# Kernel tuning notes

Hardware: AMD Instinct MI355X
Metric: run time of the kernel (lower is better)

Reference implementation:

```python
import jax, jax.numpy as jnp
import numpy as np
from jax import lax

B, T_DEC, T_ENC = 32, 400, 300
N_MEL, PRENET, ENC_D = 80, 256, 512
ATT_RNN, DEC_RNN, ATT_D = 512, 512, 128
LOC_F, LOC_K = 32, 31


def setup_inputs() -> dict:
    key = jax.random.key(0)
    ks = jax.random.split(key, 24)

    def w(k, shape):
        return jax.random.normal(k, shape, jnp.float32) / np.float32(np.sqrt(shape[-1]))

    inp = {
        "encoder_out": jax.random.normal(ks[0], (B, T_ENC, ENC_D), jnp.float32),
        "mels": jax.random.normal(ks[1], (B, T_DEC, N_MEL), jnp.float32),
        "lengths": jax.random.randint(ks[2], (B,), 1, T_ENC + 1).astype(jnp.int32),
        # prenet (3 layers, no bias)
        "W_p0": w(ks[3], (PRENET, N_MEL)),
        "W_p1": w(ks[4], (PRENET, PRENET)),
        "W_p2": w(ks[5], (PRENET, PRENET)),
        # attention GRUCell: input = prenet_dim + enc_dim = 768
        "W_ih_a": w(ks[6], (3 * ATT_RNN, PRENET + ENC_D)),
        "W_hh_a": w(ks[7], (3 * ATT_RNN, ATT_RNN)),
        "b_ih_a": jnp.zeros((3 * ATT_RNN,), jnp.float32),
        "b_hh_a": jnp.zeros((3 * ATT_RNN,), jnp.float32),
        # decoder GRUCell: input = attn_rnn + enc_dim = 1024 (what the code actually feeds)
        "W_ih_d": w(ks[8], (3 * DEC_RNN, ATT_RNN + ENC_D)),
        "W_hh_d": w(ks[9], (3 * DEC_RNN, DEC_RNN)),
        "b_ih_d": jnp.zeros((3 * DEC_RNN,), jnp.float32),
        "b_hh_d": jnp.zeros((3 * DEC_RNN,), jnp.float32),
        # location-sensitive attention
        "W_q": w(ks[10], (ATT_D, ATT_RNN)),
        "W_m": w(ks[11], (ATT_D, ENC_D)),
        "K_loc": w(ks[12], (LOC_F, 2, LOC_K)),
        "W_l": w(ks[13], (ATT_D, LOC_F)),
        "v": w(ks[14], (ATT_D,)),
        # output projection + gate
        "W_out": w(ks[15], (N_MEL, DEC_RNN + ENC_D)),
        "b_out": jnp.zeros((N_MEL,), jnp.float32),
        "W_g": w(ks[16], (1, DEC_RNN + ENC_D)),
        "b_g": jnp.zeros((1,), jnp.float32),
    }
    return inp


def _gru_cell(x, h, W_ih, W_hh, b_ih, b_hh):
    gi = x @ W_ih.T + b_ih
    gh = h @ W_hh.T + b_hh
    i_r, i_z, i_n = jnp.split(gi, 3, axis=-1)
    h_r, h_z, h_n = jnp.split(gh, 3, axis=-1)
    r = jax.nn.sigmoid(i_r + h_r)
    z = jax.nn.sigmoid(i_z + h_z)
    n = jnp.tanh(i_n + r * h_n)
    return (1.0 - z) * n + z * h


def _decoder_core(encoder_out, mels, lengths, W_p0, W_p1, W_p2,
                  W_ih_a, W_hh_a, b_ih_a, b_hh_a, W_ih_d, W_hh_d, b_ih_d, b_hh_d,
                  W_q, W_m, K_loc, W_l, v, W_out, b_out, W_g, b_g):
    Bb, T_enc, _ = encoder_out.shape
    T_dec = mels.shape[1]
    pmem = encoder_out @ W_m.T  # [B,T_enc,ATT_D], computed once
    enc_mask = jnp.arange(T_enc)[None, :] < lengths[:, None]  # [B,T_enc]
    # shifted teacher-forcing inputs: zero first frame, then mels[:, :-1]
    dec_inputs = jnp.concatenate(
        [jnp.zeros((Bb, 1, mels.shape[2]), mels.dtype), mels[:, :-1]], axis=1)
    drop_key = jax.random.key(42)
    pad = LOC_K // 2

    def prenet(x, t):
        for i, W in enumerate((W_p0, W_p1, W_p2)):
            x = jax.nn.relu(x @ W.T)
            k = jax.random.fold_in(drop_key, t * 3 + i)
            keep = jax.random.bernoulli(k, 0.5, x.shape)
            x = jnp.where(keep, x * 2.0, 0.0)  # inverted dropout p=0.5 (hardcoded training=True)
        return x

    def step(carry, xs):
        ah, dh, ctx, aw, aw_sum = carry
        frame, t = xs
        x = prenet(frame, t)
        ah = _gru_cell(jnp.concatenate([x, ctx], -1), ah, W_ih_a, W_hh_a, b_ih_a, b_hh_a)
        # location features from current + cumulative attention weights
        awc = jnp.stack([aw, aw_sum], axis=1)  # [B,2,T_enc]
        loc = lax.conv_general_dilated(awc, K_loc, (1,), [(pad, pad)],
                                       dimension_numbers=("NCH", "OIH", "NCH"))
        loc = jnp.swapaxes(loc, 1, 2) @ W_l.T  # [B,T_enc,ATT_D]
        e = jnp.tanh((ah @ W_q.T)[:, None, :] + pmem + loc) @ v  # [B,T_enc]
        e = jnp.where(enc_mask, e, -1e9)
        aw_new = jax.nn.softmax(e, axis=-1)
        ctx = jnp.einsum("bt,btd->bd", aw_new, encoder_out)
        aw_sum = aw_sum + aw_new
        dh = _gru_cell(jnp.concatenate([ah, ctx], -1), dh, W_ih_d, W_hh_d, b_ih_d, b_hh_d)
        dhc = jnp.concatenate([dh, ctx], -1)
        mel = dhc @ W_out.T + b_out  # [B,N_MEL]
        gate = (dhc @ W_g.T + b_g)[:, 0]  # [B]
        return (ah, dh, ctx, aw_new, aw_sum), (mel, gate, aw_new)

    f32 = encoder_out.dtype
    init = (jnp.zeros((Bb, ATT_RNN), f32), jnp.zeros((Bb, DEC_RNN), f32),
            jnp.zeros((Bb, ENC_D), f32), jnp.zeros((Bb, T_enc), f32),
            jnp.zeros((Bb, T_enc), f32))
    frames = jnp.swapaxes(dec_inputs, 0, 1)  # [T_dec,B,N_MEL]
    _, (mels_out, gates, aligns) = lax.scan(jax.checkpoint(step), init,
                                            (frames, jnp.arange(T_dec)))
    mel_outputs = jnp.transpose(mels_out, (1, 2, 0))  # [B,N_MEL,T_dec]
    gate_outputs = jnp.swapaxes(gates, 0, 1)          # [B,T_dec]
    alignments = jnp.swapaxes(aligns, 0, 1)           # [B,T_dec,T_enc]
    return mel_outputs, gate_outputs, alignments


def reference(encoder_out, mels, lengths, W_p0, W_p1, W_p2,
              W_ih_a, W_hh_a, b_ih_a, b_hh_a, W_ih_d, W_hh_d, b_ih_d, b_hh_d,
              W_q, W_m, K_loc, W_l, v, W_out, b_out, W_g, b_g):
    return _decoder_core(encoder_out, mels, lengths, W_p0, W_p1, W_p2,
                         W_ih_a, W_hh_a, b_ih_a, b_hh_a, W_ih_d, W_hh_d, b_ih_d, b_hh_d,
                         W_q, W_m, K_loc, W_l, v, W_out, b_out, W_g, b_g)
```

## Files before the change

kernel.cpp:

```cpp
#include <hip/hip_runtime.h>
#include <cstdint>


static constexpr int TDEC = 400, TENC = 300, NMEL = 80;
static constexpr int RING = 16;

__device__ __forceinline__ uint2 threefry2x32(uint32_t k0, uint32_t k1,
                                              uint32_t x0, uint32_t x1) {
  uint32_t k2 = k0 ^ k1 ^ 0x1BD11BDAu;
  x0 += k0; x1 += k1;
#define TFR(r) { x0 += x1; x1 = (x1 << (r)) | (x1 >> (32 - (r))); x1 ^= x0; }
  TFR(13) TFR(15) TFR(26) TFR(6)
  x0 += k1; x1 += k2 + 1u;
  TFR(17) TFR(29) TFR(16) TFR(24)
  x0 += k2; x1 += k0 + 2u;
  TFR(13) TFR(15) TFR(26) TFR(6)
  x0 += k0; x1 += k1 + 3u;
  TFR(17) TFR(29) TFR(16) TFR(24)
  x0 += k1; x1 += k2 + 4u;
  TFR(13) TFR(15) TFR(26) TFR(6)
  x0 += k2; x1 += k0 + 5u;
#undef TFR
  return make_uint2(x0, x1);
}

__device__ __forceinline__ bool keep_mask(uint32_t key0, uint32_t key1, uint32_t idx) {
  uint2 o = threefry2x32(key0, key1, 0u, idx);
  uint32_t bits = o.x ^ o.y;
  float u = __uint_as_float((bits >> 9) | 0x3f800000u) - 1.0f;
  return u < 0.5f;
}

__device__ __forceinline__ float dot4(float4 w, float4 a) {
  return w.x * a.x + w.y * a.y + w.z * a.z + w.w * a.w;
}
__device__ __forceinline__ float nt_load(const float* p) {
  return __builtin_nontemporal_load(p);
}
__device__ __forceinline__ void nt_store(float* p, float v) {
  __builtin_nontemporal_store(v, p);
}

__device__ __forceinline__ void s_rel(float* p, float v) {
  __hip_atomic_store(p, v, __ATOMIC_RELAXED, __HIP_MEMORY_SCOPE_AGENT);
}
__device__ __forceinline__ void si_rel(int* p, int v) {
  __hip_atomic_store(p, v, __ATOMIC_RELAXED, __HIP_MEMORY_SCOPE_AGENT);
}
__device__ __forceinline__ float l_rel(const float* p) {
  return __hip_atomic_load(p, __ATOMIC_RELAXED, __HIP_MEMORY_SCOPE_AGENT);
}
__device__ __forceinline__ int li_rel(const int* p) {
  return __hip_atomic_load(p, __ATOMIC_RELAXED, __HIP_MEMORY_SCOPE_AGENT);
}
__device__ __forceinline__ float4 l4(const float4* p) {
  const unsigned long long* q = (const unsigned long long*)p;
  unsigned long long a = __hip_atomic_load(q, __ATOMIC_RELAXED, __HIP_MEMORY_SCOPE_AGENT);
  unsigned long long b = __hip_atomic_load(q + 1, __ATOMIC_RELAXED, __HIP_MEMORY_SCOPE_AGENT);
  float4 r;
  ((unsigned long long*)&r)[0] = a;
  ((unsigned long long*)&r)[1] = b;
  return r;
}

__device__ __forceinline__ void wait_ge(const int* p, int tgt) {
  while (li_rel(p) < tgt) __builtin_amdgcn_s_sleep(1);
}

__device__ __forceinline__ void gsyncN(int* arrive, int* release, int id, int bno) {
  __syncthreads();
  if (id == 0) {
    if (threadIdx.x > 0 && threadIdx.x < 128)
      wait_ge(&arrive[threadIdx.x * 32], bno);
    __syncthreads();
    if (threadIdx.x < 8)
      si_rel(&release[threadIdx.x * 32], bno);
  } else {
    if (threadIdx.x == 0) {
      si_rel(&arrive[id * 32], bno);
      wait_ge(&release[(id & 7) * 32], bno);
    }
  }
  __syncthreads();
}

template <int K>
__device__ __forceinline__ void prenet_layer(const float* in_lds, float* out_lds,
                                             float* out_g, const float* __restrict__ W,
                                             uint32_t key0, uint32_t key1, int b0) {
  const int tid = threadIdx.x;
  const int cgp = tid & 63, bg = tid >> 6;
  float acc[4][4];
#pragma unroll
  for (int cc = 0; cc < 4; ++cc)
#pragma unroll
    for (int rr = 0; rr < 4; ++rr) acc[cc][rr] = 0.f;
  const float4* W4 = (const float4*)W;
  const float4* in4 = (const float4*)in_lds;
  for (int k4 = 0; k4 < K / 4; ++k4) {
    float4 a[4];
#pragma unroll
    for (int rr = 0; rr < 4; ++rr) a[rr] = in4[(bg * 4 + rr) * (K / 4) + k4];
#pragma unroll
    for (int cc = 0; cc < 4; ++cc) {
      float4 w = W4[(cgp + 64 * cc) * (K / 4) + k4];
#pragma unroll
      for (int rr = 0; rr < 4; ++rr) acc[cc][rr] += dot4(w, a[rr]);
    }
  }
#pragma unroll
  for (int cc = 0; cc < 4; ++cc)
#pragma unroll
    for (int rr = 0; rr < 4; ++rr) {
      int c = cgp + 64 * cc, br = bg * 4 + rr;
      float val = fmaxf(acc[cc][rr], 0.f);
      val = keep_mask(key0, key1, (uint32_t)((b0 + br) * 256 + c)) ? val * 2.f : 0.f;
      if (out_lds) out_lds[br * 256 + c] = val;
      if (out_g) out_g[(b0 + br) * 256 + c] = val;
    }
  __syncthreads();
}

__global__ __launch_bounds__(256) void prenet_kernel(const float* __restrict__ mels,
                                                     const float* __restrict__ Wp0,
                                                     const float* __restrict__ Wp1,
                                                     const float* __restrict__ Wp2,
                                                     float* __restrict__ x_all) {
  __shared__ float bufA[16 * 256];
  __shared__ float bufB[16 * 256];
  const int t = blockIdx.x >> 1, b0 = (blockIdx.x & 1) * 16;
  const int tid = threadIdx.x;
  for (int i = tid; i < 16 * 80; i += 256) {
    int br = i / 80, k = i % 80;
    bufB[br * 80 + k] = (t == 0) ? 0.f : mels[((b0 + br) * TDEC + (t - 1)) * NMEL + k];
  }
  __syncthreads();
  uint2 k0v = threefry2x32(0u, 42u, 0u, (uint32_t)(t * 3 + 0));
  uint2 k1v = threefry2x32(0u, 42u, 0u, (uint32_t)(t * 3 + 1));
  uint2 k2v = threefry2x32(0u, 42u, 0u, (uint32_t)(t * 3 + 2));
  prenet_layer<80>(bufB, bufA, nullptr, Wp0, k0v.x, k0v.y, b0);
  prenet_layer<256>(bufA, bufB, nullptr, Wp1, k1v.x, k1v.y, b0);
  prenet_layer<256>(bufB, nullptr, x_all + t * 8192, Wp2, k2v.x, k2v.y, b0);
}

__global__ __launch_bounds__(256) void pmem_kernel(const float* __restrict__ enc,
                                                   const float* __restrict__ Wm,
                                                   float* __restrict__ pmem) {
  const int b = blockIdx.x / 10, pc = blockIdx.x % 10;
  const int j = threadIdx.x & 127, ph = threadIdx.x >> 7;
  const float4* Wm4 = (const float4*)Wm;
  const float4* enc4 = (const float4*)enc + (size_t)(b * 300 + pc * 30 + ph * 15) * 128;
  float acc[15];
#pragma unroll
  for (int pp = 0; pp < 15; ++pp) acc[pp] = 0.f;
  for (int k4 = 0; k4 < 128; ++k4) {
    float4 w = Wm4[j * 128 + k4];
#pragma unroll
    for (int pp = 0; pp < 15; ++pp) acc[pp] += dot4(w, enc4[pp * 128 + k4]);
  }
#pragma unroll
  for (int pp = 0; pp < 15; ++pp)
    pmem[(size_t)(b * 300 + pc * 30 + ph * 15 + pp) * 128 + j] = acc[pp];
}

struct DP {
  const float *xall, *enc, *pmem;
  const int* lens;
  const float *Wiha, *Whha, *biha, *bhha;
  const float *Wihd, *Whhd, *bihd, *bhhd;
  const float *Wq, *Kloc, *Wl, *vv, *Wout, *bout, *Wg, *bg;
  float *ah, *ctxM;
  float *dh;
  float *e2;
  float *pM, *pS;
  float *V;
  float *awsum2;
  int *arrA, *relA, *arrD, *relD, *rM, *attT, *decT;
  float *omel, *ogate, *oalign;
};

__global__ __launch_bounds__(256, 1) void decoder_kernel(DP P) {
  __shared__ float4 pinW[4608];
  __shared__ float scr[6144];
  __shared__ float2 tapsL[992];
  __shared__ float pmemL[9600];
  const int tid = threadIdx.x, blk = blockIdx.x;

  if (blk < 128) {
    const int er = blk >> 2, eq = blk & 3, pb = eq * 75;
    const int idx0 = blk * 4;
    {
      const float4* Wih4 = (const float4*)P.Wiha;
      const float4* Whh4 = (const float4*)P.Whha;
      for (int i = tid; i < 2304; i += 256) {
        int g = i / 768, rem = i % 768, r2 = rem / 192, k4 = rem % 192;
        pinW[i] = Wih4[(size_t)(g * 512 + idx0 + r2) * 192 + k4];
      }
      for (int i = tid; i < 1536; i += 256) {
        int g = i / 512, rem = i % 512, r2 = rem / 128, k4 = rem % 128;
        pinW[2304 + i] = Whh4[(size_t)(g * 512 + idx0 + r2) * 128 + k4];
      }
      for (int i = tid; i < 992; i += 256) {
        int f = i / 31, k = i % 31;
        tapsL[i] = make_float2(P.Kloc[f * 62 + k], P.Kloc[f * 62 + 31 + k]);
      }
      for (int i = tid; i < 9600; i += 256) {
        int pl = i >> 7, c = i & 127;
        pmemL[pl * 128 + c] = P.pmem[((size_t)(er * 300 + pb + pl)) * 128 + c];
      }
    }
    __syncthreads();

    int bno = 0;
    for (int t = 0; t <= TDEC; ++t) {
      const int p0 = t & 1, p1 = p0 ^ 1;
      const int sc = t & (RING - 1), sp = (t - 1) & (RING - 1);
      float* ahC = P.ah + sc * 16384;
      const float* ahP = P.ah + sp * 16384;
      const float* ctxP = P.ctxM + sp * 16384;

      if ((t & 7) == 0) {
        if (tid == 0) wait_ge(P.decT, t - 4);
        __syncthreads();
      }

      if (t < TDEC) {
        const int row = tid >> 3, seg = tid & 7;
        const float4* A4p = (const float4*)(P.xall + (size_t)t * 8192);
        const float4* C4 = (const float4*)ctxP;
        const float4* H4 = (const float4*)ahP;
        float acc[24];
#pragma unroll
        for (int g = 0; g < 24; ++g) acc[g] = 0.f;
        for (int sb = 0; sb < 24; sb += 8) {
          float4 av[8];
#pragma unroll
          for (int u = 0; u < 8; ++u) {
            int k4 = (sb + u) * 8 + seg;
            av[u] = (k4 < 64) ? A4p[row * 64 + k4] : l4(&C4[row * 128 + (k4 - 64)]);
          }
#pragma unroll
          for (int u = 0; u < 8; ++u) {
            int k4 = (sb + u) * 8 + seg;
#pragma unroll
            for (int g = 0; g < 3; ++g)
#pragma unroll
              for (int i = 0; i < 4; ++i)
                acc[g * 4 + i] += dot4(pinW[(g * 4 + i) * 192 + k4], av[u]);
          }
        }
        for (int sb = 0; sb < 16; sb += 8) {
          float4 hv[8];
#pragma unroll
          for (int u = 0; u < 8; ++u) {
            int k4 = (sb + u) * 8 + seg;
            hv[u] = l4(&H4[row * 128 + k4]);
          }
#pragma unroll
          for (int u = 0; u < 8; ++u) {
            int k4 = (sb + u) * 8 + seg;
#pragma unroll
            for (int g = 0; g < 3; ++g)
#pragma unroll
              for (int i = 0; i < 4; ++i)
                acc[12 + g * 4 + i] += dot4(pinW[2304 + (g * 4 + i) * 128 + k4], hv[u]);
          }
        }
#pragma unroll
        for (int g = 0; g < 24; ++g) scr[(g * 32 + row) * 8 + seg] = acc[g];
        __syncthreads();
        if (tid < 128) {
          int i = tid >> 5, r = tid & 31;
          float gi[3], gh[3];
#pragma unroll
          for (int g = 0; g < 3; ++g) {
            float si = 0.f, sh = 0.f;
#pragma unroll
            for (int s = 0; s < 8; ++s) {
              si += scr[((g * 4 + i) * 32 + r) * 8 + s];
              sh += scr[((12 + g * 4 + i) * 32 + r) * 8 + s];
            }
            gi[g] = si + P.biha[g * 512 + idx0 + i];
            gh[g] = sh + P.bhha[g * 512 + idx0 + i];
          }
          float rr = 1.f / (1.f + expf(-(gi[0] + gh[0])));
          float zz = 1.f / (1.f + expf(-(gi[1] + gh[1])));
          float nn = tanhf(gi[2] + rr * gh[2]);
          float hp = l_rel(&ahP[r * 512 + idx0 + i]);
          s_rel(&ahC[r * 512 + idx0 + i], (1.f - zz) * nn + zz * hp);
        }
      }
      gsyncN(P.arrA, P.relA, blk, ++bno);

      {
        float* awW = scr;
        float* asW = scr + 105;
        float* convl = scr + 216;
        float* qp = scr + 2688;
        float* qb = scr + 2944;
        float* el = scr + 3072;
        float* eex = scr + 3152;
        float* ahS = scr + 3232;

        if (t < TDEC) {
          float v0s = l_rel(&ahC[er * 512 + tid]);
          float v1s = l_rel(&ahC[er * 512 + 256 + tid]);
          ahS[tid] = v0s;
          ahS[256 + tid] = v1s;
        }
        if (t >= 1) {
          float pMv[4], pSv[4];
#pragma unroll
          for (int j = 0; j < 4; ++j) pMv[j] = l_rel(&P.pM[p1 * 128 + er * 4 + j]);
#pragma unroll
          for (int j = 0; j < 4; ++j) pSv[j] = l_rel(&P.pS[p1 * 128 + er * 4 + j]);
          float M = fmaxf(fmaxf(pMv[0], pMv[1]), fmaxf(pMv[2], pMv[3]));
          float Z = 0.f;
#pragma unroll
          for (int j = 0; j < 4; ++j) Z += pSv[j] * expf(pMv[j] - M);
          float inv = 1.f / Z;
          for (int i = tid; i < 105; i += 256) {
            int p = pb - 15 + i;
            float a = 0.f, s = 0.f;
            if (p >= 0 && p < TENC) {
              float ev = l_rel(&P.e2[p1 * 9728 + er * 304 + p]);
              float sv = l_rel(&P.awsum2[p1 * 9600 + er * 300 + p]);
              a = expf(ev - M) * inv;
              s = sv + a;
            }
            awW[i] = a;
            asW[i] = s;
            if (p >= pb && p < pb + 75) {
              s_rel(&P.awsum2[p0 * 9600 + er * 300 + p], s);
              nt_store(&P.oalign[((size_t)(er * 400 + (t - 1))) * 300 + p], a);
            }
          }
        } else {
          for (int i = tid; i < 105; i += 256) { awW[i] = 0.f; asW[i] = 0.f; }
        }
        __syncthreads();

        if (t < TDEC) {
          {
            int f = tid & 31, pl0 = tid >> 5;
            for (int pl = pl0; pl < 75; pl += 8) {
              float a = 0.f;
#pragma unroll
              for (int k = 0; k < 31; ++k) {
                float2 tv = tapsL[f * 31 + k];
                a += awW[pl + k] * tv.x + asW[pl + k] * tv.y;
              }
              convl[f * 77 + pl] = a;
            }
          }
          {
            int j = tid & 127, kh = tid >> 7;
            const float4* Wq4 = (const float4*)P.Wq;
            const float4* a4 = (const float4*)ahS;
            float acc = 0.f;
            for (int k4 = kh * 64; k4 < kh * 64 + 64; ++k4)
              acc += dot4(Wq4[j * 128 + k4], a4[k4]);
            qp[j * 2 + kh] = acc;
          }
          __syncthreads();
          if (tid < 128) qb[tid] = qp[tid * 2] + qp[tid * 2 + 1];
          __syncthreads();
          {
            int w = tid >> 6, lane = tid & 63;
            float wl0[32], wl1[32];
#pragma unroll
            for (int f = 0; f < 32; ++f) {
              wl0[f] = P.Wl[lane * 32 + f];
              wl1[f] = P.Wl[(lane + 64) * 32 + f];
            }
            float v0 = P.vv[lane], v1 = P.vv[lane + 64];
            float q0 = qb[lane], q1 = qb[64 + lane];
            int len = P.lens[er];
            for (int pl = w; pl < 75; pl += 4) {
              int p = pb + pl;
              float a0 = 0.f, a1 = 0.f;
#pragma unroll
              for (int f = 0; f < 32; ++f) {
                float c = convl[f * 77 + pl];
                a0 += c * wl0[f];
                a1 += c * wl1[f];
              }
              float e0 = tanhf(q0 + pmemL[pl * 128 + lane] + a0) * v0;
              float e1 = tanhf(q1 + pmemL[pl * 128 + 64 + lane] + a1) * v1;
              float es = e0 + e1;
#pragma unroll
              for (int off = 32; off > 0; off >>= 1) es += __shfl_xor(es, off, 64);
              if (lane == 0) {
                float ev = (p < len) ? es : -1e9f;
                s_rel(&P.e2[p0 * 9728 + er * 304 + p], ev);
                el[pl] = ev;
              }
            }
          }
          __syncthreads();
          if (tid < 64) {
            int lane = tid;
            float m = -3.4e38f;
            for (int i = lane; i < 75; i += 64) m = fmaxf(m, el[i]);
#pragma unroll
            for (int off = 32; off > 0; off >>= 1) m = fmaxf(m, __shfl_xor(m, off, 64));
            float s = 0.f;
            for (int i = lane; i < 75; i += 64) {
              float x = expf(el[i] - m);
              eex[i] = x;
              s += x;
            }
#pragma unroll
            for (int off = 32; off > 0; off >>= 1) s += __shfl_xor(s, off, 64);
            if (lane == 0) {
              s_rel(&P.pM[p0 * 128 + er * 4 + eq], m);
              s_rel(&P.pS[p0 * 128 + er * 4 + eq], s);
            }
          }
          __syncthreads();
          {
            float* Vw = P.V + (size_t)p0 * 65536 + (size_t)(er * 4 + eq) * 512;
#pragma unroll
            for (int cc = 0; cc < 2; ++cc) {
              int c = tid + cc * 256;
              float acc = 0.f;
              const float* eb = P.enc + ((size_t)(er * 300 + pb)) * 512 + c;
              for (int po = 0; po < 75; ++po) acc += eex[po] * nt_load(eb + (size_t)po * 512);
              s_rel(&Vw[c], acc);
            }
          }
          __syncthreads();
          if (tid == 0) si_rel(&P.rM[(er * 4 + eq) * 32], t + 1);
          if (eq == 0) {
            if (tid < 3) wait_ge(&P.rM[(er * 4 + 1 + tid) * 32], t + 1);
            __syncthreads();
            float pMv[4], pSv[4];
#pragma unroll
            for (int j = 0; j < 4; ++j) pMv[j] = l_rel(&P.pM[p0 * 128 + er * 4 + j]);
#pragma unroll
            for (int j = 0; j < 4; ++j) pSv[j] = l_rel(&P.pS[p0 * 128 + er * 4 + j]);
            float M = fmaxf(fmaxf(pMv[0], pMv[1]), fmaxf(pMv[2], pMv[3]));
            float Z = 0.f, wq[4];
#pragma unroll
            for (int j = 0; j < 4; ++j) {
              wq[j] = expf(pMv[j] - M);
              Z += pSv[j] * wq[j];
            }
            float invZ = 1.f / Z;
            const float* Vb = P.V + (size_t)p0 * 65536 + (size_t)(er * 4) * 512;
            float* ctxC = P.ctxM + sc * 16384;
#pragma unroll
            for (int cc = 0; cc < 2; ++cc) {
              int c = tid + cc * 256;
              float vv4[4];
#pragma unroll
              for (int j = 0; j < 4; ++j) vv4[j] = l_rel(&Vb[j * 512 + c]);
              float acc = vv4[0] * wq[0] + vv4[1] * wq[1] + vv4[2] * wq[2] + vv4[3] * wq[3];
              s_rel(&ctxC[er * 512 + c], acc * invZ);
            }
          }
        }
      }
      gsyncN(P.arrA, P.relA, blk, ++bno);
      if (blk == 0 && tid == 0) si_rel(P.attT, t + 1);
    }
  } else {
    const int dblk = blk - 128;
    const int idx0 = dblk * 4;
    const int r_op = dblk >> 2, mq = dblk & 3;
    const int m0 = (mq == 0) ? 0 : 21 + 20 * (mq - 1);
    const int mcnt = (mq == 0) ? 21 : 20;
    {
      const float4* Wih4 = (const float4*)P.Wihd;
      const float4* Whh4 = (const float4*)P.Whhd;
      for (int i = tid; i < 3072; i += 256) {
        int g = i / 1024, rem = i % 1024, r2 = rem / 256, k4 = rem % 256;
        pinW[i] = Wih4[(size_t)(g * 512 + idx0 + r2) * 256 + k4];
      }
      for (int i = tid; i < 1536; i += 256) {
        int g = i / 512, rem = i % 512, r2 = rem / 128, k4 = rem % 128;
        pinW[3072 + i] = Whh4[(size_t)(g * 512 + idx0 + r2) * 128 + k4];
      }
    }
    __syncthreads();

    int bno = 0;
    for (int t = 0; t < TDEC; ++t) {
      const int p0 = t & 1, p1 = p0 ^ 1;
      const int sc = t & (RING - 1);
      const float* ahC = P.ah + sc * 16384;
      const float* ctxC = P.ctxM + sc * 16384;
      float* dhW = P.dh + p0 * 16384;
      const float* dhP = P.dh + p1 * 16384;

      if (tid == 0) wait_ge(P.attT, t + 1);
      __syncthreads();

      {
        const int row = tid >> 3, seg = tid & 7;
        const float4* A4 = (const float4*)ahC;
        const float4* C4 = (const float4*)ctxC;
        const float4* H4 = (const float4*)dhP;
        float acc[24];
#pragma unroll
        for (int g = 0; g < 24; ++g) acc[g] = 0.f;
        for (int sb = 0; sb < 32; sb += 8) {
          float4 av[8];
#pragma unroll
          for (int u = 0; u < 8; ++u) {
            int k4 = (sb + u) * 8 + seg;
            av[u] = (k4 < 128) ? l4(&A4[row * 128 + k4]) : l4(&C4[row * 128 + (k4 - 128)]);
          }
#pragma unroll
          for (int u = 0; u < 8; ++u) {
            int k4 = (sb + u) * 8 + seg;
#pragma unroll
            for (int g = 0; g < 3; ++g)
#pragma unroll
              for (int i = 0; i < 4; ++i)
                acc[g * 4 + i] += dot4(pinW[(g * 4 + i) * 256 + k4], av[u]);
          }
        }
        for (int sb = 0; sb < 16; sb += 8) {
          float4 hv[8];
#pragma unroll
          for (int u = 0; u < 8; ++u) {
            int k4 = (sb + u) * 8 + seg;
            hv[u] = l4(&H4[row * 128 + k4]);
          }
#pragma unroll
          for (int u = 0; u < 8; ++u) {
            int k4 = (sb + u) * 8 + seg;
#pragma unroll
            for (int g = 0; g < 3; ++g)
#pragma unroll
              for (int i = 0; i < 4; ++i)
                acc[12 + g * 4 + i] += dot4(pinW[3072 + (g * 4 + i) * 128 + k4], hv[u]);
          }
        }
#pragma unroll
        for (int g = 0; g < 24; ++g) scr[(g * 32 + row) * 8 + seg] = acc[g];
        __syncthreads();
        if (tid < 128) {
          int i = tid >> 5, r = tid & 31;
          float gi[3], gh[3];
#pragma unroll
          for (int g = 0; g < 3; ++g) {
            float si = 0.f, sh = 0.f;
#pragma unroll
            for (int s = 0; s < 8; ++s) {
              si += scr[((g * 4 + i) * 32 + r) * 8 + s];
              sh += scr[((12 + g * 4 + i) * 32 + r) * 8 + s];
            }
            gi[g] = si + P.bihd[g * 512 + idx0 + i];
            gh[g] = sh + P.bhhd[g * 512 + idx0 + i];
          }
          float rr = 1.f / (1.f + expf(-(gi[0] + gh[0])));
          float zz = 1.f / (1.f + expf(-(gi[1] + gh[1])));
          float nn = tanhf(gi[2] + rr * gh[2]);
          float hp = l_rel(&dhP[r * 512 + idx0 + i]);
          s_rel(&dhW[r * 512 + idx0 + i], (1.f - zz) * nn + zz * hp);
        }
      }
      gsyncN(P.arrD, P.relD, dblk, ++bno);
      if (dblk == 0 && tid == 0) si_rel(P.decT, t);

      {
        float* dhcx = scr;
        float* opl = scr + 1024;
        for (int i = tid; i < 512; i += 256) {
          float d0 = l_rel(&dhW[r_op * 512 + i]);
          float c0 = l_rel(&ctxC[r_op * 512 + i]);
          dhcx[i] = d0;
          dhcx[512 + i] = c0;
        }
        __syncthreads();
        if (tid < 2 * mcnt) {
          int m = m0 + (tid >> 1), h = tid & 1;
          const float4* W4 = (m < 80) ? ((const float4*)P.Wout + (size_t)m * 256)
                                      : (const float4*)P.Wg;
          const float4* x4 = (const float4*)dhcx;
          float a = 0.f;
          for (int k4 = h * 128; k4 < h * 128 + 128; ++k4) a += dot4(W4[k4], x4[k4]);
          opl[tid] = a;
        }
        __syncthreads();
        if (tid < mcnt) {
          int m = m0 + tid;
          float sum = opl[tid * 2] + opl[tid * 2 + 1];
          if (m < 80) nt_store(&P.omel[(size_t)(r_op * 80 + m) * 400 + t], sum + P.bout[m]);
          else nt_store(&P.ogate[r_op * 400 + t], sum + P.bg[0]);
        }
        __syncthreads();
      }
    }
  }
}

extern "C" void kernel_launch(void* const* d_in, const int* in_sizes, int n_in,
                              void* d_out, int out_size, void* d_ws, size_t ws_size,
                              hipStream_t stream) {
  const float* enc = (const float*)d_in[0];
  const float* mels = (const float*)d_in[1];
  const int* lens = (const int*)d_in[2];

  float* ws = (float*)d_ws;
  float* x_all = ws;
  float* pmem = x_all + 3276800;
  float* ah = pmem + 1228800;
  float* ctxM = ah + 262144;
  float* dh = ctxM + 262144;
  float* e2 = dh + 32768;
  float* pM = e2 + 19456;
  float* pS = pM + 256;
  float* V = pS + 256;
  float* awsum2 = V + 131072;
  int* arrA = (int*)(awsum2 + 19200);
  int* relA = arrA + 4096;
  int* arrD = relA + 256;
  int* relD = arrD + 4096;
  int* rM = relD + 256;
  int* attT = rM + 4096;
  int* decT = attT + 32;

  (void)hipMemsetAsync(ah, 0, (262144 + 262144 + 32768) * sizeof(float), stream);
  (void)hipMemsetAsync(awsum2, 0, 19200 * sizeof(float), stream);
  (void)hipMemsetAsync(arrA, 0, (4096 + 256 + 4096 + 256 + 4096 + 32 + 32) * sizeof(int),
                       stream);

  prenet_kernel<<<800, 256, 0, stream>>>(mels, (const float*)d_in[3],
                                         (const float*)d_in[4], (const float*)d_in[5],
                                         x_all);
  pmem_kernel<<<320, 256, 0, stream>>>(enc, (const float*)d_in[15], pmem);

  float* omel = (float*)d_out;
  float* ogate = omel + 32 * 80 * 400;
  float* oalign = ogate + 32 * 400;

  DP P;
  P.xall = x_all; P.enc = enc; P.pmem = pmem; P.lens = lens;
  P.Wiha = (const float*)d_in[6]; P.Whha = (const float*)d_in[7];
  P.biha = (const float*)d_in[8]; P.bhha = (const float*)d_in[9];
  P.Wihd = (const float*)d_in[10]; P.Whhd = (const float*)d_in[11];
  P.bihd = (const float*)d_in[12]; P.bhhd = (const float*)d_in[13];
  P.Wq = (const float*)d_in[14]; P.Kloc = (const float*)d_in[16];
  P.Wl = (const float*)d_in[17]; P.vv = (const float*)d_in[18];
  P.Wout = (const float*)d_in[19]; P.bout = (const float*)d_in[20];
  P.Wg = (const float*)d_in[21]; P.bg = (const float*)d_in[22];
  P.ah = ah; P.ctxM = ctxM; P.dh = dh; P.e2 = e2; P.pM = pM; P.pS = pS; P.V = V;
  P.awsum2 = awsum2;
  P.arrA = arrA; P.relA = relA; P.arrD = arrD; P.relD = relD; P.rM = rM;
  P.attT = attT; P.decT = decT;
  P.omel = omel; P.ogate = ogate; P.oalign = oalign;

  decoder_kernel<<<256, 256, 0, stream>>>(P);
}
```

Measured before the change: 42.42 ms.

## Partition GRU work by batch row and replace global barriers with per-row syncs

Reassigns GRU cells so that each group of 4 blocks owns one batch row and a quarter of the hidden units, instead of each block owning 4 hidden units across all 32 rows. This lets the 128-block grid-wide barriers be replaced with 4-block per-row barriers, and the single global progress counters with per-row counters, so rows advance independently and the lookahead window grows to 8. Weights are no longer pinned in LDS; each step reads them from global memory (relying on cache), and the row's activations are staged in LDS. The cost is much more weight traffic per step, since every block streams its weight slice each timestep.

```diff
diff --git a/kernel.cpp b/kernel.cpp
--- a/kernel.cpp
+++ b/kernel.cpp
@@ -53,32 +53,21 @@
 __device__ __forceinline__ int li_rel(const int* p) {
   return __hip_atomic_load(p, __ATOMIC_RELAXED, __HIP_MEMORY_SCOPE_AGENT);
 }
-__device__ __forceinline__ float4 l4(const float4* p) {
-  const unsigned long long* q = (const unsigned long long*)p;
-  unsigned long long a = __hip_atomic_load(q, __ATOMIC_RELAXED, __HIP_MEMORY_SCOPE_AGENT);
-  unsigned long long b = __hip_atomic_load(q + 1, __ATOMIC_RELAXED, __HIP_MEMORY_SCOPE_AGENT);
-  float4 r;
-  ((unsigned long long*)&r)[0] = a;
-  ((unsigned long long*)&r)[1] = b;
-  return r;
-}
 
 __device__ __forceinline__ void wait_ge(const int* p, int tgt) {
   while (li_rel(p) < tgt) __builtin_amdgcn_s_sleep(1);
 }
 
-__device__ __forceinline__ void gsyncN(int* arrive, int* release, int id, int bno) {
+__device__ __forceinline__ void rsync4(int* arr, int* rel, int r, int q, int val) {
   __syncthreads();
-  if (id == 0) {
-    if (threadIdx.x > 0 && threadIdx.x < 128)
-      wait_ge(&arrive[threadIdx.x * 32], bno);
+  if (q == 0) {
+    if (threadIdx.x < 3) wait_ge(&arr[(r * 4 + 1 + threadIdx.x) * 32], val);
     __syncthreads();
-    if (threadIdx.x < 8)
-      si_rel(&release[threadIdx.x * 32], bno);
+    if (threadIdx.x == 0) si_rel(&rel[r * 32], val);
   } else {
     if (threadIdx.x == 0) {
-      si_rel(&arrive[id * 32], bno);
-      wait_ge(&release[(id & 7) * 32], bno);
+      si_rel(&arr[(r * 4 + q) * 32], val);
+      wait_ge(&rel[r * 32], val);
     }
   }
   __syncthreads();
@@ -175,43 +164,38 @@
   float *pM, *pS;
   float *V;
   float *awsum2;
-  int *arrA, *relA, *arrD, *relD, *rM, *attT, *decT;
+  int *arrA, *relA, *arrD, *relD, *rM, *attRow, *decRow;
   float *omel, *ogate, *oalign;
 };
 
 __global__ __launch_bounds__(256, 1) void decoder_kernel(DP P) {
-  __shared__ float4 pinW[4608];
   __shared__ float scr[6144];
+  __shared__ float stg[1536];
   __shared__ float2 tapsL[992];
   __shared__ float pmemL[9600];
   const int tid = threadIdx.x, blk = blockIdx.x;
-
-  if (blk < 128) {
-    const int er = blk >> 2, eq = blk & 3, pb = eq * 75;
-    const int idx0 = blk * 4;
-    {
-      const float4* Wih4 = (const float4*)P.Wiha;
-      const float4* Whh4 = (const float4*)P.Whha;
-      for (int i = tid; i < 2304; i += 256) {
-        int g = i / 768, rem = i % 768, r2 = rem / 192, k4 = rem % 192;
-        pinW[i] = Wih4[(size_t)(g * 512 + idx0 + r2) * 192 + k4];
-      }
-      for (int i = tid; i < 1536; i += 256) {
-        int g = i / 512, rem = i % 512, r2 = rem / 128, k4 = rem % 128;
-        pinW[2304 + i] = Whh4[(size_t)(g * 512 + idx0 + r2) * 128 + k4];
-      }
-      for (int i = tid; i < 992; i += 256) {
-        int f = i / 31, k = i % 31;
-        tapsL[i] = make_float2(P.Kloc[f * 62 + k], P.Kloc[f * 62 + 31 + k]);
-      }
-      for (int i = tid; i < 9600; i += 256) {
-        int pl = i >> 7, c = i & 127;
-        pmemL[pl * 128 + c] = P.pmem[((size_t)(er * 300 + pb + pl)) * 128 + c];
-      }
+  const bool isAtt = (blk < 128);
+  const int lb = isAtt ? blk : (blk - 128);
+  const int r = lb >> 2, q = lb & 3;
+  const int pb = q * 75;
+  const int hg = tid >> 3, seg = tid & 7;
+
+  if (isAtt) {
+    for (int i = tid; i < 992; i += 256) {
+      int f = i / 31, k = i % 31;
+      tapsL[i] = make_float2(P.Kloc[f * 62 + k], P.Kloc[f * 62 + 31 + k]);
     }
-    __syncthreads();
-
-    int bno = 0;
+    for (int i = tid; i < 9600; i += 256) {
+      int pl = i >> 7, c = i & 127;
+      pmemL[pl * 128 + c] = P.pmem[((size_t)(r * 300 + pb + pl)) * 128 + c];
+    }
+  }
+  __syncthreads();
+
+  if (isAtt) {
+    float* xS = stg;
+    float* cS = stg + 256;
+    float* hS = stg + 768;
     for (int t = 0; t <= TDEC; ++t) {
       const int p0 = t & 1, p1 = p0 ^ 1;
       const int sc = t & (RING - 1), sp = (t - 1) & (RING - 1);
@@ -220,77 +204,76 @@
       const float* ctxP = P.ctxM + sp * 16384;
 
       if ((t & 7) == 0) {
-        if (tid == 0) wait_ge(P.decT, t - 4);
+        if (tid == 0) wait_ge(&P.decRow[r * 32], t - 8);
         __syncthreads();
       }
 
       if (t < TDEC) {
-        const int row = tid >> 3, seg = tid & 7;
-        const float4* A4p = (const float4*)(P.xall + (size_t)t * 8192);
-        const float4* C4 = (const float4*)ctxP;
-        const float4* H4 = (const float4*)ahP;
+        {
+          float xv = P.xall[(size_t)t * 8192 + r * 256 + tid];
+          float c0 = l_rel(&ctxP[r * 512 + tid]);
+          float c1 = l_rel(&ctxP[r * 512 + 256 + tid]);
+          float h0 = l_rel(&ahP[r * 512 + tid]);
+          float h1 = l_rel(&ahP[r * 512 + 256 + tid]);
+          xS[tid] = xv;
+          cS[tid] = c0; cS[256 + tid] = c1;
+          hS[tid] = h0; hS[256 + tid] = h1;
+        }
+        __syncthreads();
+        const float4* xS4 = (const float4*)xS;
+        const float4* cS4 = (const float4*)cS;
+        const float4* hS4 = (const float4*)hS;
+        const float4* Wih4 = (const float4*)P.Wiha;
+        const float4* Whh4 = (const float4*)P.Whha;
         float acc[24];
 #pragma unroll
         for (int g = 0; g < 24; ++g) acc[g] = 0.f;
-        for (int sb = 0; sb < 24; sb += 8) {
-          float4 av[8];
-#pragma unroll
-          for (int u = 0; u < 8; ++u) {
-            int k4 = (sb + u) * 8 + seg;
-            av[u] = (k4 < 64) ? A4p[row * 64 + k4] : l4(&C4[row * 128 + (k4 - 64)]);
-          }
-#pragma unroll
-          for (int u = 0; u < 8; ++u) {
-            int k4 = (sb + u) * 8 + seg;
-#pragma unroll
-            for (int g = 0; g < 3; ++g)
-#pragma unroll
-              for (int i = 0; i < 4; ++i)
-                acc[g * 4 + i] += dot4(pinW[(g * 4 + i) * 192 + k4], av[u]);
-          }
-        }
-        for (int sb = 0; sb < 16; sb += 8) {
-          float4 hv[8];
-#pragma unroll
-          for (int u = 0; u < 8; ++u) {
-            int k4 = (sb + u) * 8 + seg;
-            hv[u] = l4(&H4[row * 128 + k4]);
-          }
-#pragma unroll
-          for (int u = 0; u < 8; ++u) {
-            int k4 = (sb + u) * 8 + seg;
-#pragma unroll
-            for (int g = 0; g < 3; ++g)
-#pragma unroll
-              for (int i = 0; i < 4; ++i)
-                acc[12 + g * 4 + i] += dot4(pinW[2304 + (g * 4 + i) * 128 + k4], hv[u]);
-          }
-        }
-#pragma unroll
-        for (int g = 0; g < 24; ++g) scr[(g * 32 + row) * 8 + seg] = acc[g];
+        for (int s = 0; s < 24; ++s) {
+          int k4 = s * 8 + seg;
+          float4 a = (k4 < 64) ? xS4[k4] : cS4[k4 - 64];
+#pragma unroll
+          for (int g = 0; g < 3; ++g)
+#pragma unroll
+            for (int i = 0; i < 4; ++i)
+              acc[g * 4 + i] +=
+                  dot4(Wih4[(size_t)(g * 512 + q * 128 + hg * 4 + i) * 192 + k4], a);
+        }
+        for (int s = 0; s < 16; ++s) {
+          int k4 = s * 8 + seg;
+          float4 h = hS4[k4];
+#pragma unroll
+          for (int g = 0; g < 3; ++g)
+#pragma unroll
+            for (int i = 0; i < 4; ++i)
+              acc[12 + g * 4 + i] +=
+                  dot4(Whh4[(size_t)(g * 512 + q * 128 + hg * 4 + i) * 128 + k4], h);
+        }
+        __syncthreads();
+#pragma unroll
+        for (int g = 0; g < 24; ++g) scr[(g * 32 + hg) * 8 + seg] = acc[g];
         __syncthreads();
         if (tid < 128) {
-          int i = tid >> 5, r = tid & 31;
+          int hglob = q * 128 + tid;
           float gi[3], gh[3];
 #pragma unroll
           for (int g = 0; g < 3; ++g) {
             float si = 0.f, sh = 0.f;
 #pragma unroll
             for (int s = 0; s < 8; ++s) {
-              si += scr[((g * 4 + i) * 32 + r) * 8 + s];
-              sh += scr[((12 + g * 4 + i) * 32 + r) * 8 + s];
-            }
-            gi[g] = si + P.biha[g * 512 + idx0 + i];
-            gh[g] = sh + P.bhha[g * 512 + idx0 + i];
+              si += scr[((g * 4 + (tid & 3)) * 32 + (tid >> 2)) * 8 + s];
+              sh += scr[((12 + g * 4 + (tid & 3)) * 32 + (tid >> 2)) * 8 + s];
+            }
+            gi[g] = si + P.biha[g * 512 + hglob];
+            gh[g] = sh + P.bhha[g * 512 + hglob];
           }
           float rr = 1.f / (1.f + expf(-(gi[0] + gh[0])));
           float zz = 1.f / (1.f + expf(-(gi[1] + gh[1])));
           float nn = tanhf(gi[2] + rr * gh[2]);
-          float hp = l_rel(&ahP[r * 512 + idx0 + i]);
-          s_rel(&ahC[r * 512 + idx0 + i], (1.f - zz) * nn + zz * hp);
+          float hp = hS[q * 128 + tid];
+          s_rel(&ahC[r * 512 + q * 128 + tid], (1.f - zz) * nn + zz * hp);
         }
       }
-      gsyncN(P.arrA, P.relA, blk, ++bno);
+      rsync4(P.arrA, P.relA, r, q, 2 * t + 1);
 
       {
         float* awW = scr;
@@ -303,17 +286,17 @@
         float* ahS = scr + 3232;
 
         if (t < TDEC) {
-          float v0s = l_rel(&ahC[er * 512 + tid]);
-          float v1s = l_rel(&ahC[er * 512 + 256 + tid]);
+          float v0s = l_rel(&ahC[r * 512 + tid]);
+          float v1s = l_rel(&ahC[r * 512 + 256 + tid]);
           ahS[tid] = v0s;
           ahS[256 + tid] = v1s;
         }
         if (t >= 1) {
           float pMv[4], pSv[4];
 #pragma unroll
-          for (int j = 0; j < 4; ++j) pMv[j] = l_rel(&P.pM[p1 * 128 + er * 4 + j]);
-#pragma unroll
-          for (int j = 0; j < 4; ++j) pSv[j] = l_rel(&P.pS[p1 * 128 + er * 4 + j]);
+          for (int j = 0; j < 4; ++j) pMv[j] = l_rel(&P.pM[p1 * 128 + r * 4 + j]);
+#pragma unroll
+          for (int j = 0; j < 4; ++j) pSv[j] = l_rel(&P.pS[p1 * 128 + r * 4 + j]);
           float M = fmaxf(fmaxf(pMv[0], pMv[1]), fmaxf(pMv[2], pMv[3]));
           float Z = 0.f;
 #pragma unroll
@@ -323,16 +306,16 @@
             int p = pb - 15 + i;
             float a = 0.f, s = 0.f;
             if (p >= 0 && p < TENC) {
-              float ev = l_rel(&P.e2[p1 * 9728 + er * 304 + p]);
-              float sv = l_rel(&P.awsum2[p1 * 9600 + er * 300 + p]);
+              float ev = l_rel(&P.e2[p1 * 9728 + r * 304 + p]);
+              float sv = l_rel(&P.awsum2[p1 * 9600 + r * 300 + p]);
               a = expf(ev - M) * inv;
               s = sv + a;
             }
             awW[i] = a;
             asW[i] = s;
             if (p >= pb && p < pb + 75) {
-              s_rel(&P.awsum2[p0 * 9600 + er * 300 + p], s);
-              nt_store(&P.oalign[((size_t)(er * 400 + (t - 1))) * 300 + p], a);
+              s_rel(&P.awsum2[p0 * 9600 + r * 300 + p], s);
+              nt_store(&P.oalign[((size_t)(r * 400 + (t - 1))) * 300 + p], a);
             }
           }
         } else {
@@ -375,7 +358,7 @@
             }
             float v0 = P.vv[lane], v1 = P.vv[lane + 64];
             float q0 = qb[lane], q1 = qb[64 + lane];
-            int len = P.lens[er];
+            int len = P.lens[r];
             for (int pl = w; pl < 75; pl += 4) {
               int p = pb + pl;
               float a0 = 0.f, a1 = 0.f;
@@ -392,7 +375,7 @@
               for (int off = 32; off > 0; off >>= 1) es += __shfl_xor(es, off, 64);
               if (lane == 0) {
                 float ev = (p < len) ? es : -1e9f;
-                s_rel(&P.e2[p0 * 9728 + er * 304 + p], ev);
+                s_rel(&P.e2[p0 * 9728 + r * 304 + p], ev);
                 el[pl] = ev;
               }
             }
@@ -413,32 +396,32 @@
 #pragma unroll
             for (int off = 32; off > 0; off >>= 1) s += __shfl_xor(s, off, 64);
             if (lane == 0) {
-              s_rel(&P.pM[p0 * 128 + er * 4 + eq], m);
-              s_rel(&P.pS[p0 * 128 + er * 4 + eq], s);
+              s_rel(&P.pM[p0 * 128 + r * 4 + q], m);
+              s_rel(&P.pS[p0 * 128 + r * 4 + q], s);
             }
           }
           __syncthreads();
           {
-            float* Vw = P.V + (size_t)p0 * 65536 + (size_t)(er * 4 + eq) * 512;
+            float* Vw = P.V + (size_t)p0 * 65536 + (size_t)(r * 4 + q) * 512;
 #pragma unroll
             for (int cc = 0; cc < 2; ++cc) {
               int c = tid + cc * 256;
               float acc = 0.f;
-              const float* eb = P.enc + ((size_t)(er * 300 + pb)) * 512 + c;
+              const float* eb = P.enc + ((size_t)(r * 300 + pb)) * 512 + c;
               for (int po = 0; po < 75; ++po) acc += eex[po] * nt_load(eb + (size_t)po * 512);
               s_rel(&Vw[c], acc);
             }
           }
           __syncthreads();
-          if (tid == 0) si_rel(&P.rM[(er * 4 + eq) * 32], t + 1);
-          if (eq == 0) {
-            if (tid < 3) wait_ge(&P.rM[(er * 4 + 1 + tid) * 32], t + 1);
+          if (tid == 0) si_rel(&P.rM[(r * 4 + q) * 32], t + 1);
+          if (q == 0) {
+            if (tid < 3) wait_ge(&P.rM[(r * 4 + 1 + tid) * 32], t + 1);
             __syncthreads();
             float pMv[4], pSv[4];
 #pragma unroll
-            for (int j = 0; j < 4; ++j) pMv[j] = l_rel(&P.pM[p0 * 128 + er * 4 + j]);
-#pragma unroll
-            for (int j = 0; j < 4; ++j) pSv[j] = l_rel(&P.pS[p0 * 128 + er * 4 + j]);
+            for (int j = 0; j < 4; ++j) pMv[j] = l_rel(&P.pM[p0 * 128 + r * 4 + j]);
+#pragma unroll
+            for (int j = 0; j < 4; ++j) pSv[j] = l_rel(&P.pS[p0 * 128 + r * 4 + j]);
             float M = fmaxf(fmaxf(pMv[0], pMv[1]), fmaxf(pMv[2], pMv[3]));
             float Z = 0.f, wq[4];
 #pragma unroll
@@ -447,7 +430,7 @@
               Z += pSv[j] * wq[j];
             }
             float invZ = 1.f / Z;
-            const float* Vb = P.V + (size_t)p0 * 65536 + (size_t)(er * 4) * 512;
+            const float* Vb = P.V + (size_t)p0 * 65536 + (size_t)(r * 4) * 512;
             float* ctxC = P.ctxM + sc * 16384;
 #pragma unroll
             for (int cc = 0; cc < 2; ++cc) {
@@ -456,35 +439,20 @@
 #pragma unroll
               for (int j = 0; j < 4; ++j) vv4[j] = l_rel(&Vb[j * 512 + c]);
               float acc = vv4[0] * wq[0] + vv4[1] * wq[1] + vv4[2] * wq[2] + vv4[3] * wq[3];
-              s_rel(&ctxC[er * 512 + c], acc * invZ);
+              s_rel(&ctxC[r * 512 + c], acc * invZ);
             }
           }
         }
       }
-      gsyncN(P.arrA, P.relA, blk, ++bno);
-      if (blk == 0 && tid == 0) si_rel(P.attT, t + 1);
+      rsync4(P.arrA, P.relA, r, q, 2 * t + 2);
+      if (q == 0 && tid == 0) si_rel(&P.attRow[r * 32], t + 1);
     }
   } else {
-    const int dblk = blk - 128;
-    const int idx0 = dblk * 4;
-    const int r_op = dblk >> 2, mq = dblk & 3;
-    const int m0 = (mq == 0) ? 0 : 21 + 20 * (mq - 1);
-    const int mcnt = (mq == 0) ? 21 : 20;
-    {
-      const float4* Wih4 = (const float4*)P.Wihd;
-      const float4* Whh4 = (const float4*)P.Whhd;
-      for (int i = tid; i < 3072; i += 256) {
-        int g = i / 1024, rem = i % 1024, r2 = rem / 256, k4 = rem % 256;
-        pinW[i] = Wih4[(size_t)(g * 512 + idx0 + r2) * 256 + k4];
-      }
-      for (int i = tid; i < 1536; i += 256) {
-        int g = i / 512, rem = i % 512, r2 = rem / 128, k4 = rem % 128;
-        pinW[3072 + i] = Whh4[(size_t)(g * 512 + idx0 + r2) * 128 + k4];
-      }
-    }
-    __syncthreads();
-
-    int bno = 0;
+    float* aS = stg;
+    float* cS = stg + 512;
+    float* hS = stg + 1024;
+    const int m0 = (q == 0) ? 0 : 21 + 20 * (q - 1);
+    const int mcnt = (q == 0) ? 21 : 20;
     for (int t = 0; t < TDEC; ++t) {
       const int p0 = t & 1, p1 = p0 ^ 1;
       const int sc = t & (RING - 1);
@@ -493,103 +461,107 @@
       float* dhW = P.dh + p0 * 16384;
       const float* dhP = P.dh + p1 * 16384;
 
-      if (tid == 0) wait_ge(P.attT, t + 1);
+      if (tid == 0) wait_ge(&P.attRow[r * 32], t + 1);
       __syncthreads();
 
       {
-        const int row = tid >> 3, seg = tid & 7;
-        const float4* A4 = (const float4*)ahC;
-        const float4* C4 = (const float4*)ctxC;
-        const float4* H4 = (const float4*)dhP;
+        float a0 = l_rel(&ahC[r * 512 + tid]);
+        float a1 = l_rel(&ahC[r * 512 + 256 + tid]);
+        float c0 = l_rel(&ctxC[r * 512 + tid]);
+        float c1 = l_rel(&ctxC[r * 512 + 256 + tid]);
+        float h0 = l_rel(&dhP[r * 512 + tid]);
+        float h1 = l_rel(&dhP[r * 512 + 256 + tid]);
+        aS[tid] = a0; aS[256 + tid] = a1;
+        cS[tid] = c0; cS[256 + tid] = c1;
+        hS[tid] = h0; hS[256 + tid] = h1;
+      }
+      __syncthreads();
+      {
+        const float4* aS4 = (const float4*)aS;
+        const float4* cS4 = (const float4*)cS;
+        const float4* hS4 = (const float4*)hS;
+        const float4* Wih4 = (const float4*)P.Wihd;
+        const float4* Whh4 = (const float4*)P.Whhd;
         float acc[24];
 #pragma unroll
         for (int g = 0; g < 24; ++g) acc[g] = 0.f;
-        for (int sb = 0; sb < 32; sb += 8) {
-          float4 av[8];
-#pragma unroll
-          for (int u = 0; u < 8; ++u) {
-            int k4 = (sb + u) * 8 + seg;
-            av[u] = (k4 < 128) ? l4(&A4[row * 128 + k4]) : l4(&C4[row * 128 + (k4 - 128)]);
-          }
-#pragma unroll
-          for (int u = 0; u < 8; ++u) {
-            int k4 = (sb + u) * 8 + seg;
-#pragma unroll
-            for (int g = 0; g < 3; ++g)
-#pragma unroll
-              for (int i = 0; i < 4; ++i)
-                acc[g * 4 + i] += dot4(pinW[(g * 4 + i) * 256 + k4], av[u]);
-          }
-        }
-        for (int sb = 0; sb < 16; sb += 8) {
-          float4 hv[8];
-#pragma unroll
-          for (int u = 0; u < 8; ++u) {
-            int k4 = (sb + u) * 8 + seg;
-            hv[u] = l4(&H4[row * 128 + k4]);
-          }
-#pragma unroll
-          for (int u = 0; u < 8; ++u) {
-            int k4 = (sb + u) * 8 + seg;
-#pragma unroll
-            for (int g = 0; g < 3; ++g)
-#pragma unroll
-              for (int i = 0; i < 4; ++i)
-                acc[12 + g * 4 + i] += dot4(pinW[3072 + (g * 4 + i) * 128 + k4], hv[u]);
-          }
-        }
-#pragma unroll
-        for (int g = 0; g < 24; ++g) scr[(g * 32 + row) * 8 + seg] = acc[g];
+        for (int s = 0; s < 32; ++s) {
+          int k4 = s * 8 + seg;
+          float4 a = (k4 < 128) ? aS4[k4] : cS4[k4 - 128];
+#pragma unroll
+          for (int g = 0; g < 3; ++g)
+#pragma unroll
+            for (int i = 0; i < 4; ++i)
+              acc[g * 4 + i] +=
+                  dot4(Wih4[(size_t)(g * 512 + q * 128 + hg * 4 + i) * 256 + k4], a);
+        }
+        for (int s = 0; s < 16; ++s) {
+          int k4 = s * 8 + seg;
+          float4 h = hS4[k4];
+#pragma unroll
+          for (int g = 0; g < 3; ++g)
+#pragma unroll
+            for (int i = 0; i < 4; ++i)
+              acc[12 + g * 4 + i] +=
+                  dot4(Whh4[(size_t)(g * 512 + q * 128 + hg * 4 + i) * 128 + k4], h);
+        }
+        __syncthreads();
+#pragma unroll
+        for (int g = 0; g < 24; ++g) scr[(g * 32 + hg) * 8 + seg] = acc[g];
         __syncthreads();
         if (tid < 128) {
-          int i = tid >> 5, r = tid & 31;
+          int hglob = q * 128 + tid;
           float gi[3], gh[3];
 #pragma unroll
           for (int g = 0; g < 3; ++g) {
             float si = 0.f, sh = 0.f;
 #pragma unroll
             for (int s = 0; s < 8; ++s) {
-              si += scr[((g * 4 + i) * 32 + r) * 8 + s];
-              sh += scr[((12 + g * 4 + i) * 32 + r) * 8 + s];
-            }
-            gi[g] = si + P.bihd[g * 512 + idx0 + i];
-            gh[g] = sh + P.bhhd[g * 512 + idx0 + i];
+              si += scr[((g * 4 + (tid & 3)) * 32 + (tid >> 2)) * 8 + s];
+              sh += scr[((12 + g * 4 + (tid & 3)) * 32 + (tid >> 2)) * 8 + s];
+            }
+            gi[g] = si + P.bihd[g * 512 + hglob];
+            gh[g] = sh + P.bhhd[g * 512 + hglob];
           }
           float rr = 1.f / (1.f + expf(-(gi[0] + gh[0])));
           float zz = 1.f / (1.f + expf(-(gi[1] + gh[1])));
           float nn = tanhf(gi[2] + rr * gh[2]);
-          float hp = l_rel(&dhP[r * 512 + idx0 + i]);
-          s_rel(&dhW[r * 512 + idx0 + i], (1.f - zz) * nn + zz * hp);
+          float hp = hS[q * 128 + tid];
+          s_rel(&dhW[r * 512 + q * 128 + tid], (1.f - zz) * nn + zz * hp);
         }
       }
-      gsyncN(P.arrD, P.relD, dblk, ++bno);
-      if (dblk == 0 && tid == 0) si_rel(P.decT, t);
+      rsync4(P.arrD, P.relD, r, q, t + 1);
+      if (q == 0 && tid == 0) si_rel(&P.decRow[r * 32], t + 1);
 
       {
-        float* dhcx = scr;
-        float* opl = scr + 1024;
-        for (int i = tid; i < 512; i += 256) {
-          float d0 = l_rel(&dhW[r_op * 512 + i]);
-          float c0 = l_rel(&ctxC[r_op * 512 + i]);
-          dhcx[i] = d0;
-          dhcx[512 + i] = c0;
+        float* dhS = scr;
+        float* opl = scr + 512;
+        {
+          float d0 = l_rel(&dhW[r * 512 + tid]);
+          float d1 = l_rel(&dhW[r * 512 + 256 + tid]);
+          dhS[tid] = d0;
+          dhS[256 + tid] = d1;
         }
         __syncthreads();
         if (tid < 2 * mcnt) {
           int m = m0 + (tid >> 1), h = tid & 1;
           const float4* W4 = (m < 80) ? ((const float4*)P.Wout + (size_t)m * 256)
                                       : (const float4*)P.Wg;
-          const float4* x4 = (const float4*)dhcx;
+          const float4* d4 = (const float4*)dhS;
+          const float4* c4 = (const float4*)cS;
           float a = 0.f;
-          for (int k4 = h * 128; k4 < h * 128 + 128; ++k4) a += dot4(W4[k4], x4[k4]);
+          for (int k4 = h * 128; k4 < h * 128 + 128; ++k4) {
+            float4 x = (k4 < 128) ? d4[k4] : c4[k4 - 128];
+            a += dot4(W4[k4], x);
+          }
           opl[tid] = a;
         }
         __syncthreads();
         if (tid < mcnt) {
           int m = m0 + tid;
           float sum = opl[tid * 2] + opl[tid * 2 + 1];
-          if (m < 80) nt_store(&P.omel[(size_t)(r_op * 80 + m) * 400 + t], sum + P.bout[m]);
-          else nt_store(&P.ogate[r_op * 400 + t], sum + P.bg[0]);
+          if (m < 80) nt_store(&P.omel[(size_t)(r * 80 + m) * 400 + t], sum + P.bout[m]);
+          else nt_store(&P.ogate[r * 400 + t], sum + P.bg[0]);
         }
         __syncthreads();
       }
@@ -617,15 +589,16 @@
   float* awsum2 = V + 131072;
   int* arrA = (int*)(awsum2 + 19200);
   int* relA = arrA + 4096;
-  int* arrD = relA + 256;
+  int* arrD = relA + 1024;
   int* relD = arrD + 4096;
-  int* rM = relD + 256;
-  int* attT = rM + 4096;
-  int* decT = attT + 32;
+  int* rM = relD + 1024;
+  int* attRow = rM + 4096;
+  int* decRow = attRow + 1024;
 
   (void)hipMemsetAsync(ah, 0, (262144 + 262144 + 32768) * sizeof(float), stream);
   (void)hipMemsetAsync(awsum2, 0, 19200 * sizeof(float), stream);
-  (void)hipMemsetAsync(arrA, 0, (4096 + 256 + 4096 + 256 + 4096 + 32 + 32) * sizeof(int),
+  (void)hipMemsetAsync(arrA, 0,
+                       (4096 + 1024 + 4096 + 1024 + 4096 + 1024 + 1024) * sizeof(int),
                        stream);
 
   prenet_kernel<<<800, 256, 0, stream>>>(mels, (const float*)d_in[3],
@@ -650,7 +623,7 @@
   P.ah = ah; P.ctxM = ctxM; P.dh = dh; P.e2 = e2; P.pM = pM; P.pS = pS; P.V = V;
   P.awsum2 = awsum2;
   P.arrA = arrA; P.relA = relA; P.arrD = arrD; P.relD = relD; P.rM = rM;
-  P.attT = attT; P.decT = decT;
+  P.attRow = attRow; P.decRow = decRow;
   P.omel = omel; P.ogate = ogate; P.oalign = oalign;
 
   decoder_kernel<<<256, 256, 0, stream>>>(P);
```

Result: slower. 64.82 ms (+52.8%).
